# Kernel tuning notes

Hardware: AMD Instinct MI355X
Metric: run time of the kernel (lower is better)

The kernel has to match this reference:

```python
import jax, jax.numpy as jnp
import numpy as np

D = 1024
B, T = 4, 2048


def setup_inputs() -> dict:
    key = jax.random.key(0)
    ks = jax.random.split(key, 7)
    s = 0.02
    return {
        "x": jax.random.normal(ks[0], (B, T, D), dtype=jnp.float32),
        "W_in": s * jax.random.normal(ks[1], (2 * D, D), dtype=jnp.float32),
        "b_in": jnp.zeros((2 * D,), dtype=jnp.float32),
        "W_s": s * jax.random.normal(ks[2], (D, D), dtype=jnp.float32),
        "b_s": jnp.zeros((D,), dtype=jnp.float32),
        "W_o": s * jax.random.normal(ks[3], (D, D), dtype=jnp.float32),
        "b_o": jnp.zeros((D,), dtype=jnp.float32),
    }


def _scan_combine(c1, c2):
    # h_t = a_t * h_{t-1} + b_t  -> associative composition of affine maps
    a1, b1 = c1
    a2, b2 = c2
    return a2 * a1, a2 * b1 + b2


def reference(x, W_in, b_in, W_s, b_s, W_o, b_o):
    # Batched projections over all timesteps (h-independent)
    gv = jnp.einsum("btd,ed->bte", x, W_in) + b_in          # [B,T,2D]
    gate = jax.nn.sigmoid(gv[..., :D])                        # [B,T,D]
    val = gv[..., D:]                                         # [B,T,D]
    sv = jnp.tanh(jnp.einsum("btd,ed->bte", val, W_s) + b_s)  # [B,T,D]
    # Linear recurrence h_t = (1-gate_t)*h_{t-1} + gate_t*sv_t, h_0 = 0
    a = 1.0 - gate
    b = gate * sv
    _, h = jax.lax.associative_scan(_scan_combine, (a, b), axis=1)  # h: [B,T,D]
    out = jnp.einsum("btd,ed->bte", h, W_o) + b_o
    return x + out
```

## Files before the change

### kernel.cpp

```cpp
#include <hip/hip_runtime.h>
#include <hip/hip_bf16.h>
#include <cmath>

#define B_DIM 4
#define T_DIM 2048
#define D_DIM 1024
#define M_DIM 8192
#define KP    2048

#define NCH   64
#define CHL   32

using bf16 = __hip_bfloat16;
typedef __attribute__((ext_vector_type(8))) short frag8;
typedef __attribute__((ext_vector_type(4))) float f32x4;

#define XS_OFF   0L
#define WIN_OFF  33554432L
#define WSS_OFF  37748736L
#define WOS_OFF  39845888L
#define GATE_OFF 41943040L
#define VS_OFF   75497472L
#define AF_OFF   92274688L
#define BF_OFF   125829120L
#define ACH_OFF  159383552L
#define BCH_OFF  160432128L
#define CAR_OFF  161480704L

__global__ void split_kernel(const float* __restrict__ src, bf16* __restrict__ dst, long total4) {
    long i4 = (long)blockIdx.x * blockDim.x + threadIdx.x;
    if (i4 >= total4) return;
    long i = i4 * 4;
    const float4 v = *(const float4*)&src[i];
    long r = i >> 10;
    int  c = (int)(i & 1023);
    ushort hi[4], lo[4];
    const float vv[4] = {v.x, v.y, v.z, v.w};
#pragma unroll
    for (int j = 0; j < 4; ++j) {
        bf16 h = __float2bfloat16(vv[j]);
        hi[j] = *(ushort*)&h;
        bf16 l2 = __float2bfloat16(vv[j] - __bfloat162float(h));
        lo[j] = *(ushort*)&l2;
    }
    *(ushort4*)&dst[r * KP + c]        = make_ushort4(hi[0], hi[1], hi[2], hi[3]);
    *(ushort4*)&dst[r * KP + c + 1024] = make_ushort4(lo[0], lo[1], lo[2], lo[3]);
}

__global__ void split_hi_kernel(const float* __restrict__ src, bf16* __restrict__ dst, long total4) {
    long i4 = (long)blockIdx.x * blockDim.x + threadIdx.x;
    if (i4 >= total4) return;
    long i = i4 * 4;
    const float4 v = *(const float4*)&src[i];
    bf16 h0 = __float2bfloat16(v.x), h1 = __float2bfloat16(v.y);
    bf16 h2 = __float2bfloat16(v.z), h3 = __float2bfloat16(v.w);
    *(ushort4*)&dst[i] = make_ushort4(*(ushort*)&h0, *(ushort*)&h1, *(ushort*)&h2, *(ushort*)&h3);
}

#define AS1 const __attribute__((address_space(1))) void*
#define AS3 __attribute__((address_space(3))) void*

template<int EPI, int NTT, int LDA>
__global__ __launch_bounds__(256, 2)
void gemm128(const bf16* __restrict__ A, const bf16* __restrict__ Bw,
             const float* __restrict__ bias,
             const float* __restrict__ gatef_in,
             const float* __restrict__ x_in,
             float* __restrict__ out0, float* __restrict__ out1,
             bf16* __restrict__ outv)
{
    __shared__ bf16 As[4][4096];
    __shared__ bf16 Bs[4][4096];
    const int t  = threadIdx.x;
    const int l  = t & 63;
    const int w  = t >> 6;
    const int wr = w >> 1, wc = w & 1;
    const int bm = blockIdx.x;
    const int bn = blockIdx.y;

    f32x4 acc[4][4] = {};

    const int sr  = t >> 2;
    const int sg  = (sr & 3) ^ ((sr >> 2) & 3);
    const int scS = ((t & 3) * 8) ^ (sg << 3);
    const bf16* Ab = A  + ((long)bm * 128 + sr) * LDA  + scS;
    const bf16* Bb = Bw + ((long)bn * 128 + sr) * 1024 + scS;

    const int rk    = (((l >> 4) ^ (l & 3) ^ ((l >> 2) & 3)) << 3);
    const int rowA0 = wr * 64 + (l & 15);
    const int rowB0 = wc * 64 + (l & 15);

#define STAGE(kt) {                                                                \
    const int  s_ = (kt) & 3;                                                      \
    const long ka = (long)(kt) * 32;                                               \
    const long kb = (long)((kt) & 31) * 32;                                        \
    __builtin_amdgcn_global_load_lds((AS1)(Ab + ka),             (AS3)&As[s_][t * 8],        16, 0, 0); \
    __builtin_amdgcn_global_load_lds((AS1)(Ab + 64 * LDA + ka),  (AS3)&As[s_][2048 + t * 8], 16, 0, 0); \
    __builtin_amdgcn_global_load_lds((AS1)(Bb + kb),             (AS3)&Bs[s_][t * 8],        16, 0, 0); \
    __builtin_amdgcn_global_load_lds((AS1)(Bb + 64 * 1024 + kb), (AS3)&Bs[s_][2048 + t * 8], 16, 0, 0); \
}

    STAGE(0); STAGE(1); STAGE(2);
    asm volatile("s_waitcnt vmcnt(8)" ::: "memory");
    __builtin_amdgcn_s_barrier();
    asm volatile("" ::: "memory");

    for (int kt = 0; kt < NTT; ++kt) {
        const int s = kt & 3;
        frag8 fb0 = *(const frag8*)&Bs[s][(rowB0     ) * 32 + rk];
        frag8 fb1 = *(const frag8*)&Bs[s][(rowB0 + 16) * 32 + rk];
        frag8 fb2 = *(const frag8*)&Bs[s][(rowB0 + 32) * 32 + rk];
        frag8 fb3 = *(const frag8*)&Bs[s][(rowB0 + 48) * 32 + rk];
        frag8 fa0 = *(const frag8*)&As[s][(rowA0     ) * 32 + rk];
        frag8 fa1 = *(const frag8*)&As[s][(rowA0 + 16) * 32 + rk];
        frag8 fa2 = *(const frag8*)&As[s][(rowA0 + 32) * 32 + rk];
        frag8 fa3 = *(const frag8*)&As[s][(rowA0 + 48) * 32 + rk];
        if (kt + 3 < NTT) STAGE(kt + 3);
        __builtin_amdgcn_s_setprio(1);
        acc[0][0] = __builtin_amdgcn_mfma_f32_16x16x32_bf16(fa0, fb0, acc[0][0], 0, 0, 0);
        acc[0][1] = __builtin_amdgcn_mfma_f32_16x16x32_bf16(fa0, fb1, acc[0][1], 0, 0, 0);
        acc[0][2] = __builtin_amdgcn_mfma_f32_16x16x32_bf16(fa0, fb2, acc[0][2], 0, 0, 0);
        acc[0][3] = __builtin_amdgcn_mfma_f32_16x16x32_bf16(fa0, fb3, acc[0][3], 0, 0, 0);
        acc[1][0] = __builtin_amdgcn_mfma_f32_16x16x32_bf16(fa1, fb0, acc[1][0], 0, 0, 0);
        acc[1][1] = __builtin_amdgcn_mfma_f32_16x16x32_bf16(fa1, fb1, acc[1][1], 0, 0, 0);
        acc[1][2] = __builtin_amdgcn_mfma_f32_16x16x32_bf16(fa1, fb2, acc[1][2], 0, 0, 0);
        acc[1][3] = __builtin_amdgcn_mfma_f32_16x16x32_bf16(fa1, fb3, acc[1][3], 0, 0, 0);
        acc[2][0] = __builtin_amdgcn_mfma_f32_16x16x32_bf16(fa2, fb0, acc[2][0], 0, 0, 0);
        acc[2][1] = __builtin_amdgcn_mfma_f32_16x16x32_bf16(fa2, fb1, acc[2][1], 0, 0, 0);
        acc[2][2] = __builtin_amdgcn_mfma_f32_16x16x32_bf16(fa2, fb2, acc[2][2], 0, 0, 0);
        acc[2][3] = __builtin_amdgcn_mfma_f32_16x16x32_bf16(fa2, fb3, acc[2][3], 0, 0, 0);
        acc[3][0] = __builtin_amdgcn_mfma_f32_16x16x32_bf16(fa3, fb0, acc[3][0], 0, 0, 0);
        acc[3][1] = __builtin_amdgcn_mfma_f32_16x16x32_bf16(fa3, fb1, acc[3][1], 0, 0, 0);
        acc[3][2] = __builtin_amdgcn_mfma_f32_16x16x32_bf16(fa3, fb2, acc[3][2], 0, 0, 0);
        acc[3][3] = __builtin_amdgcn_mfma_f32_16x16x32_bf16(fa3, fb3, acc[3][3], 0, 0, 0);
        __builtin_amdgcn_s_setprio(0);
        asm volatile("" ::: "memory");
        if (kt < NTT - 3)       { asm volatile("s_waitcnt vmcnt(8)" ::: "memory"); }
        else if (kt == NTT - 3) { asm volatile("s_waitcnt vmcnt(4)" ::: "memory"); }
        else if (kt == NTT - 2) { asm volatile("s_waitcnt vmcnt(0)" ::: "memory"); }
        __builtin_amdgcn_s_barrier();
        asm volatile("" ::: "memory");
    }
#undef STAGE

    const int r4 = (l >> 4) * 4;
    const int cl = l & 15;
#pragma unroll
    for (int fm = 0; fm < 4; ++fm) {
#pragma unroll
        for (int fn = 0; fn < 4; ++fn) {
            const int n = bn * 128 + wc * 64 + fn * 16 + cl;
            const float bn_bias = bias[n];
#pragma unroll
            for (int j = 0; j < 4; ++j) {
                const int m = bm * 128 + wr * 64 + fm * 16 + r4 + j;
                float v = acc[fm][fn][j] + bn_bias;
                if (EPI == 1) {
                    if (n < 1024) {
                        out0[(long)m * 1024 + n] = 1.0f / (1.0f + expf(-v));
                    } else {
                        outv[(long)m * 1024 + (n - 1024)] = __float2bfloat16(v);
                    }
                } else if (EPI == 2) {
                    const float sv = tanhf(v);
                    const float g  = gatef_in[(long)m * 1024 + n];
                    out0[(long)m * 1024 + n] = 1.0f - g;
                    out1[(long)m * 1024 + n] = g * sv;
                } else {
                    out0[(long)m * 1024 + n] = x_in[(long)m * 1024 + n] + v;
                }
            }
        }
    }
}

__global__ void scan_phase1(const float* __restrict__ af, const float* __restrict__ bfv,
                            float* __restrict__ Ach, float* __restrict__ Bch) {
    int tid = blockIdx.x * 256 + threadIdx.x;
    int c = tid >> 12;
    int r = tid & 4095;
    int bi = r >> 10;
    long base = ((long)bi * T_DIM + c * CHL) * D_DIM + (r & 1023);
    float A = 1.0f, Bc = 0.0f;
#pragma unroll 4
    for (int i = 0; i < CHL; ++i) {
        float a = af[base + (long)i * D_DIM];
        float b = bfv[base + (long)i * D_DIM];
        A *= a;
        Bc = a * Bc + b;
    }
    Ach[tid] = A;
    Bch[tid] = Bc;
}

__global__ void scan_phase2(const float* __restrict__ Ach, const float* __restrict__ Bch,
                            float* __restrict__ carry) {
    int r = blockIdx.x * 256 + threadIdx.x;
    float h = 0.0f;
#pragma unroll
    for (int c = 0; c < NCH; ++c) {
        carry[c * 4096 + r] = h;
        h = Ach[c * 4096 + r] * h + Bch[c * 4096 + r];
    }
}

__global__ void scan_phase3(const float* __restrict__ af, const float* __restrict__ bfv,
                            const float* __restrict__ carry, bf16* __restrict__ Hs) {
    int tid = blockIdx.x * 256 + threadIdx.x;
    int c = tid >> 12;
    int r = tid & 4095;
    int bi = r >> 10;
    int d  = r & 1023;
    long base = ((long)bi * T_DIM + c * CHL) * D_DIM + d;
    float h = carry[tid];
#pragma unroll 4
    for (int i = 0; i < CHL; ++i) {
        float a = af[base + (long)i * D_DIM];
        float b = bfv[base + (long)i * D_DIM];
        h = a * h + b;
        long m = (long)bi * T_DIM + c * CHL + i;
        Hs[m * 1024 + d] = __float2bfloat16(h);
    }
}

extern "C" void kernel_launch(void* const* d_in, const int* in_sizes, int n_in,
                              void* d_out, int out_size, void* d_ws, size_t ws_size,
                              hipStream_t stream) {
    const float* x   = (const float*)d_in[0];
    const float* Win = (const float*)d_in[1];
    const float* bin = (const float*)d_in[2];
    const float* Wsm = (const float*)d_in[3];
    const float* bs  = (const float*)d_in[4];
    const float* Wo  = (const float*)d_in[5];
    const float* bo  = (const float*)d_in[6];
    float* out = (float*)d_out;
    char*  ws  = (char*)d_ws;

    bf16*  Xs    = (bf16*)(ws + XS_OFF);
    bf16*  Wins  = (bf16*)(ws + WIN_OFF);
    bf16*  Wss   = (bf16*)(ws + WSS_OFF);
    bf16*  Wos   = (bf16*)(ws + WOS_OFF);
    float* gatef = (float*)(ws + GATE_OFF);
    bf16*  Vs    = (bf16*)(ws + VS_OFF);
    float* af    = (float*)(ws + AF_OFF);
    float* bfv   = (float*)(ws + BF_OFF);
    float* Ach   = (float*)(ws + ACH_OFF);
    float* Bch   = (float*)(ws + BCH_OFF);
    float* car   = (float*)(ws + CAR_OFF);
    bf16*  Hs    = (bf16*)(ws + XS_OFF);

    split_kernel   <<<(M_DIM * D_DIM / 4 + 255) / 256, 256, 0, stream>>>(x,   Xs,   (long)M_DIM * D_DIM / 4);
    split_hi_kernel<<<(2048 * 1024 / 4 + 255) / 256,  256, 0, stream>>>(Win, Wins, 2048L * 1024 / 4);
    split_hi_kernel<<<(1024 * 1024 / 4 + 255) / 256,  256, 0, stream>>>(Wsm, Wss,  1024L * 1024 / 4);
    split_hi_kernel<<<(1024 * 1024 / 4 + 255) / 256,  256, 0, stream>>>(Wo,  Wos,  1024L * 1024 / 4);

    dim3 g1(M_DIM / 128, 2048 / 128);
    gemm128<1, 64, 2048><<<g1, 256, 0, stream>>>(Xs, Wins, bin, nullptr, nullptr, gatef, nullptr, Vs);

    dim3 g2(M_DIM / 128, 1024 / 128);
    gemm128<2, 32, 1024><<<g2, 256, 0, stream>>>(Vs, Wss, bs, gatef, nullptr, af, bfv, nullptr);

    scan_phase1<<<NCH * 4096 / 256, 256, 0, stream>>>(af, bfv, Ach, Bch);
    scan_phase2<<<4096 / 256, 256, 0, stream>>>(Ach, Bch, car);
    scan_phase3<<<NCH * 4096 / 256, 256, 0, stream>>>(af, bfv, car, Hs);

    gemm128<3, 32, 1024><<<g2, 256, 0, stream>>>(Hs, Wos, bo, nullptr, x, out, nullptr, nullptr);
}
```

Measured before the change: 311.4 us.

## Cut GEMM pipeline to 3 stages, merge weight conversions and scan phases

Result: faster. 302.2 us (-3.0%).

```diff
diff --git a/kernel.cpp b/kernel.cpp
--- a/kernel.cpp
+++ b/kernel.cpp
@@ -25,7 +25,6 @@
 #define BF_OFF   125829120L
 #define ACH_OFF  159383552L
 #define BCH_OFF  160432128L
-#define CAR_OFF  161480704L
 
 __global__ void split_kernel(const float* __restrict__ src, bf16* __restrict__ dst, long total4) {
     long i4 = (long)blockIdx.x * blockDim.x + threadIdx.x;
@@ -47,10 +46,16 @@
     *(ushort4*)&dst[r * KP + c + 1024] = make_ushort4(lo[0], lo[1], lo[2], lo[3]);
 }
 
-__global__ void split_hi_kernel(const float* __restrict__ src, bf16* __restrict__ dst, long total4) {
-    long i4 = (long)blockIdx.x * blockDim.x + threadIdx.x;
-    if (i4 >= total4) return;
-    long i = i4 * 4;
+__global__ void wconv_kernel(const float* __restrict__ Win, const float* __restrict__ Wsm,
+                             const float* __restrict__ Wo,
+                             bf16* __restrict__ Wins, bf16* __restrict__ Wss,
+                             bf16* __restrict__ Wos) {
+    long i4 = (long)blockIdx.x * 256 + threadIdx.x;
+    const float* src; bf16* dst; long off;
+    if (i4 < 524288)      { src = Win; dst = Wins; off = i4; }
+    else if (i4 < 786432) { src = Wsm; dst = Wss;  off = i4 - 524288; }
+    else                  { src = Wo;  dst = Wos;  off = i4 - 786432; }
+    long i = off * 4;
     const float4 v = *(const float4*)&src[i];
     bf16 h0 = __float2bfloat16(v.x), h1 = __float2bfloat16(v.y);
     bf16 h2 = __float2bfloat16(v.z), h3 = __float2bfloat16(v.w);
@@ -61,7 +66,7 @@
 #define AS3 __attribute__((address_space(3))) void*
 
 template<int EPI, int NTT, int LDA>
-__global__ __launch_bounds__(256, 2)
+__global__ __launch_bounds__(256, 3)
 void gemm128(const bf16* __restrict__ A, const bf16* __restrict__ Bw,
              const float* __restrict__ bias,
              const float* __restrict__ gatef_in,
@@ -69,8 +74,8 @@
              float* __restrict__ out0, float* __restrict__ out1,
              bf16* __restrict__ outv)
 {
-    __shared__ bf16 As[4][4096];
-    __shared__ bf16 Bs[4][4096];
+    __shared__ bf16 As[3][4096];
+    __shared__ bf16 Bs[3][4096];
     const int t  = threadIdx.x;
     const int l  = t & 63;
     const int w  = t >> 6;
@@ -90,32 +95,31 @@
     const int rowA0 = wr * 64 + (l & 15);
     const int rowB0 = wc * 64 + (l & 15);
 
-#define STAGE(kt) {                                                                \
-    const int  s_ = (kt) & 3;                                                      \
+#define STAGE(slot, kt) {                                                          \
     const long ka = (long)(kt) * 32;                                               \
     const long kb = (long)((kt) & 31) * 32;                                        \
-    __builtin_amdgcn_global_load_lds((AS1)(Ab + ka),             (AS3)&As[s_][t * 8],        16, 0, 0); \
-    __builtin_amdgcn_global_load_lds((AS1)(Ab + 64 * LDA + ka),  (AS3)&As[s_][2048 + t * 8], 16, 0, 0); \
-    __builtin_amdgcn_global_load_lds((AS1)(Bb + kb),             (AS3)&Bs[s_][t * 8],        16, 0, 0); \
-    __builtin_amdgcn_global_load_lds((AS1)(Bb + 64 * 1024 + kb), (AS3)&Bs[s_][2048 + t * 8], 16, 0, 0); \
-}
-
-    STAGE(0); STAGE(1); STAGE(2);
-    asm volatile("s_waitcnt vmcnt(8)" ::: "memory");
+    __builtin_amdgcn_global_load_lds((AS1)(Ab + ka),             (AS3)&As[slot][t * 8],        16, 0, 0); \
+    __builtin_amdgcn_global_load_lds((AS1)(Ab + 64 * LDA + ka),  (AS3)&As[slot][2048 + t * 8], 16, 0, 0); \
+    __builtin_amdgcn_global_load_lds((AS1)(Bb + kb),             (AS3)&Bs[slot][t * 8],        16, 0, 0); \
+    __builtin_amdgcn_global_load_lds((AS1)(Bb + 64 * 1024 + kb), (AS3)&Bs[slot][2048 + t * 8], 16, 0, 0); \
+}
+
+    STAGE(0, 0); STAGE(1, 1);
+    asm volatile("s_waitcnt vmcnt(4)" ::: "memory");
     __builtin_amdgcn_s_barrier();
     asm volatile("" ::: "memory");
 
+    int sR = 0, sS = 2;
     for (int kt = 0; kt < NTT; ++kt) {
-        const int s = kt & 3;
-        frag8 fb0 = *(const frag8*)&Bs[s][(rowB0     ) * 32 + rk];
-        frag8 fb1 = *(const frag8*)&Bs[s][(rowB0 + 16) * 32 + rk];
-        frag8 fb2 = *(const frag8*)&Bs[s][(rowB0 + 32) * 32 + rk];
-        frag8 fb3 = *(const frag8*)&Bs[s][(rowB0 + 48) * 32 + rk];
-        frag8 fa0 = *(const frag8*)&As[s][(rowA0     ) * 32 + rk];
-        frag8 fa1 = *(const frag8*)&As[s][(rowA0 + 16) * 32 + rk];
-        frag8 fa2 = *(const frag8*)&As[s][(rowA0 + 32) * 32 + rk];
-        frag8 fa3 = *(const frag8*)&As[s][(rowA0 + 48) * 32 + rk];
-        if (kt + 3 < NTT) STAGE(kt + 3);
+        frag8 fb0 = *(const frag8*)&Bs[sR][(rowB0     ) * 32 + rk];
+        frag8 fb1 = *(const frag8*)&Bs[sR][(rowB0 + 16) * 32 + rk];
+        frag8 fb2 = *(const frag8*)&Bs[sR][(rowB0 + 32) * 32 + rk];
+        frag8 fb3 = *(const frag8*)&Bs[sR][(rowB0 + 48) * 32 + rk];
+        frag8 fa0 = *(const frag8*)&As[sR][(rowA0     ) * 32 + rk];
+        frag8 fa1 = *(const frag8*)&As[sR][(rowA0 + 16) * 32 + rk];
+        frag8 fa2 = *(const frag8*)&As[sR][(rowA0 + 32) * 32 + rk];
+        frag8 fa3 = *(const frag8*)&As[sR][(rowA0 + 48) * 32 + rk];
+        if (kt + 2 < NTT) STAGE(sS, kt + 2);
         __builtin_amdgcn_s_setprio(1);
         acc[0][0] = __builtin_amdgcn_mfma_f32_16x16x32_bf16(fa0, fb0, acc[0][0], 0, 0, 0);
         acc[0][1] = __builtin_amdgcn_mfma_f32_16x16x32_bf16(fa0, fb1, acc[0][1], 0, 0, 0);
@@ -135,11 +139,12 @@
         acc[3][3] = __builtin_amdgcn_mfma_f32_16x16x32_bf16(fa3, fb3, acc[3][3], 0, 0, 0);
         __builtin_amdgcn_s_setprio(0);
         asm volatile("" ::: "memory");
-        if (kt < NTT - 3)       { asm volatile("s_waitcnt vmcnt(8)" ::: "memory"); }
-        else if (kt == NTT - 3) { asm volatile("s_waitcnt vmcnt(4)" ::: "memory"); }
+        if (kt < NTT - 2)       { asm volatile("s_waitcnt vmcnt(4)" ::: "memory"); }
         else if (kt == NTT - 2) { asm volatile("s_waitcnt vmcnt(0)" ::: "memory"); }
         __builtin_amdgcn_s_barrier();
         asm volatile("" ::: "memory");
+        sR = (sR == 2) ? 0 : sR + 1;
+        sS = (sS == 2) ? 0 : sS + 1;
     }
 #undef STAGE
 
@@ -193,26 +198,18 @@
     Bch[tid] = Bc;
 }
 
-__global__ void scan_phase2(const float* __restrict__ Ach, const float* __restrict__ Bch,
-                            float* __restrict__ carry) {
-    int r = blockIdx.x * 256 + threadIdx.x;
-    float h = 0.0f;
-#pragma unroll
-    for (int c = 0; c < NCH; ++c) {
-        carry[c * 4096 + r] = h;
-        h = Ach[c * 4096 + r] * h + Bch[c * 4096 + r];
-    }
-}
-
-__global__ void scan_phase3(const float* __restrict__ af, const float* __restrict__ bfv,
-                            const float* __restrict__ carry, bf16* __restrict__ Hs) {
+__global__ void scan_phase23(const float* __restrict__ af, const float* __restrict__ bfv,
+                             const float* __restrict__ Ach, const float* __restrict__ Bch,
+                             bf16* __restrict__ Hs) {
     int tid = blockIdx.x * 256 + threadIdx.x;
     int c = tid >> 12;
     int r = tid & 4095;
     int bi = r >> 10;
     int d  = r & 1023;
+    float h = 0.0f;
+    for (int j = 0; j < c; ++j)
+        h = Ach[j * 4096 + r] * h + Bch[j * 4096 + r];
     long base = ((long)bi * T_DIM + c * CHL) * D_DIM + d;
-    float h = carry[tid];
 #pragma unroll 4
     for (int i = 0; i < CHL; ++i) {
         float a = af[base + (long)i * D_DIM];
@@ -246,13 +243,10 @@
     float* bfv   = (float*)(ws + BF_OFF);
     float* Ach   = (float*)(ws + ACH_OFF);
     float* Bch   = (float*)(ws + BCH_OFF);
-    float* car   = (float*)(ws + CAR_OFF);
     bf16*  Hs    = (bf16*)(ws + XS_OFF);
 
-    split_kernel   <<<(M_DIM * D_DIM / 4 + 255) / 256, 256, 0, stream>>>(x,   Xs,   (long)M_DIM * D_DIM / 4);
-    split_hi_kernel<<<(2048 * 1024 / 4 + 255) / 256,  256, 0, stream>>>(Win, Wins, 2048L * 1024 / 4);
-    split_hi_kernel<<<(1024 * 1024 / 4 + 255) / 256,  256, 0, stream>>>(Wsm, Wss,  1024L * 1024 / 4);
-    split_hi_kernel<<<(1024 * 1024 / 4 + 255) / 256,  256, 0, stream>>>(Wo,  Wos,  1024L * 1024 / 4);
+    split_kernel<<<(M_DIM * D_DIM / 4 + 255) / 256, 256, 0, stream>>>(x, Xs, (long)M_DIM * D_DIM / 4);
+    wconv_kernel<<<4096, 256, 0, stream>>>(Win, Wsm, Wo, Wins, Wss, Wos);
 
     dim3 g1(M_DIM / 128, 2048 / 128);
     gemm128<1, 64, 2048><<<g1, 256, 0, stream>>>(Xs, Wins, bin, nullptr, nullptr, gatef, nullptr, Vs);
@@ -260,9 +254,8 @@
     dim3 g2(M_DIM / 128, 1024 / 128);
     gemm128<2, 32, 1024><<<g2, 256, 0, stream>>>(Vs, Wss, bs, gatef, nullptr, af, bfv, nullptr);
 
-    scan_phase1<<<NCH * 4096 / 256, 256, 0, stream>>>(af, bfv, Ach, Bch);
-    scan_phase2<<<4096 / 256, 256, 0, stream>>>(Ach, Bch, car);
-    scan_phase3<<<NCH * 4096 / 256, 256, 0, stream>>>(af, bfv, car, Hs);
+    scan_phase1 <<<NCH * 4096 / 256, 256, 0, stream>>>(af, bfv, Ach, Bch);
+    scan_phase23<<<NCH * 4096 / 256, 256, 0, stream>>>(af, bfv, Ach, Bch, Hs);
 
     gemm128<3, 32, 1024><<<g2, 256, 0, stream>>>(Hs, Wos, bo, nullptr, x, out, nullptr, nullptr);
 }
```
